# Kernel optimization log

Hardware: AMD Instinct MI355X
Metric: run time of the kernel (lower is better)

Reference implementation:

```python
import jax, jax.numpy as jnp
import numpy as np

N_TH = 32
HIDDEN = 128
BETA = 0.9
THRESH = 0.5
SCALE = 25.0
LN_EPS = 1e-5


def _spike(x):
    # forward of FastSigmoid surrogate: Heaviside
    return (x > 0).astype(x.dtype)


def _layernorm(h, g, b):
    mu = jnp.mean(h, axis=-1, keepdims=True)
    var = jnp.var(h, axis=-1, keepdims=True)
    return (h - mu) * jax.lax.rsqrt(var + LN_EPS) * g + b


def setup_inputs() -> dict:
    key = jax.random.key(0)
    ks = jax.random.split(key, 6)
    B, T = 2048, 512
    in_dim = 4 * N_TH  # 128
    x = jax.random.normal(ks[0], (B, T, 4), dtype=jnp.float32)
    W_in = jax.random.normal(ks[1], (HIDDEN, in_dim), dtype=jnp.float32) / np.sqrt(in_dim)
    b_in = jnp.zeros((HIDDEN,), dtype=jnp.float32)
    ln_g = jnp.ones((HIDDEN,), dtype=jnp.float32)
    ln_b = jnp.zeros((HIDDEN,), dtype=jnp.float32)
    W_out = jax.random.normal(ks[2], (2, HIDDEN), dtype=jnp.float32) / np.sqrt(HIDDEN)
    b_out = jnp.zeros((2,), dtype=jnp.float32)
    return {"x": x, "W_in": W_in, "b_in": b_in, "ln_g": ln_g,
            "ln_b": ln_b, "W_out": W_out, "b_out": b_out}


def reference(x, W_in, b_in, ln_g, ln_b, W_out, b_out):
    B, T, _ = x.shape
    thresholds = jnp.linspace(-3.0, 3.0, N_TH, dtype=x.dtype)  # [N_TH]
    sigma = 5.0 / N_TH
    # Gaussian threshold encoding for all 4 channels at once: [B,T,4,N_TH]
    enc = jnp.exp(-0.5 * (x[..., None] - thresholds) ** 2 / sigma ** 2)
    spikes_in = enc.reshape(B, T, 4 * N_TH)  # concat order matches channel-major
    spikes_tbd = jnp.transpose(spikes_in, (1, 0, 2))  # [T,B,128]

    mem0 = jnp.zeros((B, HIDDEN), dtype=x.dtype)
    ro0 = jnp.zeros((B, 2), dtype=x.dtype)

    def step(carry, s_t):
        mem, ro = carry
        curr = _layernorm(s_t @ W_in.T + b_in, ln_g, ln_b)
        # dropout is identity in eval mode
        mem = mem * BETA + curr * (1.0 - BETA)
        spk = _spike(mem - THRESH)
        mem = mem - spk * THRESH
        ro = ro + spk @ W_out.T + b_out
        return (mem, ro), None

    (_, readout), _ = jax.lax.scan(step, (mem0, ro0), spikes_tbd)
    return readout  # [B,2]
```

## Files before the change

### kernel.cpp

```cpp
#include <hip/hip_runtime.h>
#include <math.h>

#define HID 128
#define TT 32

typedef __attribute__((ext_vector_type(8))) short short8v;
typedef __attribute__((ext_vector_type(16))) float f32x16;

template<int CTRL, int RMASK>
__device__ __forceinline__ float dpp_add_stage(float v) {
  int s = __builtin_amdgcn_update_dpp(0, __float_as_int(v), CTRL, RMASK, 0xf, true);
  return v + __int_as_float(s);
}
__device__ __forceinline__ float wave_red_sum(float v) {
  v = dpp_add_stage<0x111, 0xf>(v);
  v = dpp_add_stage<0x112, 0xf>(v);
  v = dpp_add_stage<0x114, 0xf>(v);
  v = dpp_add_stage<0x118, 0xf>(v);
  v = dpp_add_stage<0x142, 0xa>(v);
  v = dpp_add_stage<0x143, 0xc>(v);
  return __int_as_float(__builtin_amdgcn_readlane(__float_as_int(v), 63));
}

#define REP8(F) F(0) F(1) F(2) F(3) F(4) F(5) F(6) F(7)

__device__ __forceinline__ void encode_tile(
    int tid2, int tile, unsigned int* Eh, unsigned int* El,
    const float* __restrict__ xb) {
  const int t5 = tid2 >> 2;
  const int ch = tid2 & 3;
  const float coef = (float)(-0.5 * 1024.0 / 25.0);
  float xc = xb[(tile * TT + t5) * 4 + ch];
#pragma unroll
  for (int c2 = 0; c2 < 4; ++c2) {
    unsigned int hi4[4], lo4[4];
#pragma unroll
    for (int p = 0; p < 4; ++p) {
      int j0 = c2 * 8 + p * 2;
      float th0 = fmaf((float)j0, 6.0f / 31.0f, -3.0f);
      float th1 = fmaf((float)(j0 + 1), 6.0f / 31.0f, -3.0f);
      float d0 = xc - th0, d1 = xc - th1;
      float e0 = __expf(coef * d0 * d0);
      float e1 = __expf(coef * d1 * d1);
      unsigned u0 = __float_as_uint(e0) + 0x8000u;
      unsigned u1 = __float_as_uint(e1) + 0x8000u;
      hi4[p] = __builtin_amdgcn_perm(u1, u0, 0x07060302u);
      float l0 = e0 - __uint_as_float(u0 & 0xffff0000u);
      float l1 = e1 - __uint_as_float(u1 & 0xffff0000u);
      unsigned v0 = __float_as_uint(l0) + 0x8000u;
      unsigned v1 = __float_as_uint(l1) + 0x8000u;
      lo4[p] = __builtin_amdgcn_perm(v1, v0, 0x07060302u);
    }
    int chunk = ch * 4 + c2;
    int idx = t5 * 64 + (((chunk ^ t5) & 15) << 2);
    *(uint4*)&Eh[idx] = make_uint4(hi4[0], hi4[1], hi4[2], hi4[3]);
    *(uint4*)&El[idx] = make_uint4(lo4[0], lo4[1], lo4[2], lo4[3]);
  }
}

__global__ __launch_bounds__(256) __attribute__((amdgpu_waves_per_eu(3, 3)))
void snn_mfma_kernel(
    const float* __restrict__ x, const float* __restrict__ Win,
    const float* __restrict__ b_in, const float* __restrict__ ln_g,
    const float* __restrict__ ln_b, const float* __restrict__ Wout,
    const float* __restrict__ b_out, float* __restrict__ out, int T) {
  __shared__ unsigned int Ebuf[2][TT * 64];
  __shared__ float Hn[TT * HID];
  __shared__ float red[256];
  __shared__ float bias_lds[HID];

  const int tid = threadIdx.x;
  const int w   = tid >> 6;
  const int l   = tid & 63;
  const int hh  = l >> 5;
  const int l31 = l & 31;
  const int b   = blockIdx.x;
  const int ntiles = T / TT;
  const float* xb = x + (size_t)b * (size_t)T * 4;

  const float* wrow = Win + (size_t)(32 * w + l31) * HID + hh * 8;
#define LDW(kt) short8v wh##kt, wl##kt; { \
    float tmp[8]; \
    *(float4*)&tmp[0] = *(const float4*)(wrow + (kt) * 16); \
    *(float4*)&tmp[4] = *(const float4*)(wrow + (kt) * 16 + 4); \
    _Pragma("unroll") \
    for (int e = 0; e < 8; ++e) { \
      unsigned u = __float_as_uint(tmp[e]) + 0x8000u; \
      wh##kt[e] = (short)(u >> 16); \
      float lof = tmp[e] - __uint_as_float(u & 0xffff0000u); \
      wl##kt[e] = (short)((__float_as_uint(lof) + 0x8000u) >> 16); \
    } }
  REP8(LDW)
#undef LDW

  const int srow = tid & 127;
  const float gr10 = 0.1f * ln_g[srow];
  const float br10 = 0.1f * ln_b[srow];
  const float wo0x2 = 2.0f * Wout[srow];
  const float wo1x2 = 2.0f * Wout[HID + srow];
  float mem = 0.f, cnt = 0.f;

  if (tid < 128) bias_lds[tid] = b_in[tid];
  else           encode_tile(tid - 128, 0, &Ebuf[0][0], &Ebuf[1][0], xb);
  __syncthreads();

  const unsigned int* Eh = &Ebuf[0][0];
  const unsigned int* El = &Ebuf[1][0];
  const int t5 = l31;

  for (int tau = 0; tau < ntiles; ++tau) {
#define RDB(kt) \
    short8v bh##kt = *(const short8v*)&Eh[t5 * 64 + ((((2 * (kt) + hh) ^ t5) & 15) << 2)]; \
    short8v bl##kt = *(const short8v*)&El[t5 * 64 + ((((2 * (kt) + hh) ^ t5) & 15) << 2)];

    f32x16 accA = {}, accB = {};
#define MM(kt) { RDB(kt) \
    accA = __builtin_amdgcn_mfma_f32_32x32x16_bf16(wh##kt, bh##kt, accA, 0, 0, 0); \
    accB = __builtin_amdgcn_mfma_f32_32x32x16_bf16(wh##kt, bl##kt, accB, 0, 0, 0); \
    accB = __builtin_amdgcn_mfma_f32_32x32x16_bf16(wl##kt, bh##kt, accB, 0, 0, 0); }
    REP8(MM)
#undef MM
#undef RDB

    float bb[16];
    {
      const int rb = 32 * w + 4 * hh;
      *(float4*)&bb[0]  = *(const float4*)&bias_lds[rb];
      *(float4*)&bb[4]  = *(const float4*)&bias_lds[rb + 8];
      *(float4*)&bb[8]  = *(const float4*)&bias_lds[rb + 16];
      *(float4*)&bb[12] = *(const float4*)&bias_lds[rb + 24];
    }
    float s1 = 0.f, s2 = 0.f;
#pragma unroll
    for (int r = 0; r < 16; ++r) {
      float hrv = (accA[r] + accB[r]) + bb[r];
      accA[r] = hrv;
      s1 += hrv;
      s2 = fmaf(hrv, hrv, s2);
    }
    s1 += __shfl_xor(s1, 32);
    s2 += __shfl_xor(s2, 32);
    if (l < 32) *(float2*)&red[w * 64 + 2 * l31] = make_float2(s1, s2);
    __syncthreads();

    float2 q0 = *(const float2*)&red[0 + 2 * l31];
    float2 q1 = *(const float2*)&red[64 + 2 * l31];
    float2 q2 = *(const float2*)&red[128 + 2 * l31];
    float2 q3 = *(const float2*)&red[192 + 2 * l31];
    float S1 = (q0.x + q1.x) + (q2.x + q3.x);
    float S2 = (q0.y + q1.y) + (q2.y + q3.y);
    float mu = S1 * (1.0f / 128.0f);
    float var = S2 * (1.0f / 128.0f) - mu * mu;
    float rstd = 1.0f / sqrtf(var + 1e-5f);
    float sh = -mu * rstd;

#pragma unroll
    for (int r = 0; r < 16; ++r) {
      int row = 32 * w + 4 * hh + (r & 3) + 8 * (r >> 2);
      Hn[t5 * 128 + (row ^ t5)] = fmaf(accA[r], rstd, sh);
    }
    __syncthreads();

    if (tid < 128) {
#pragma unroll 8
      for (int tt = 0; tt < TT; ++tt) {
        float hn = Hn[tt * 128 + (tid ^ tt)];
        float cc = fmaf(hn, gr10, br10);
        mem = fmaf(mem, 0.9f, cc);
        float d = (mem > 0.5f) ? 0.5f : 0.0f;
        mem -= d;
        cnt += d;
      }
    } else if (tau + 1 < ntiles) {
      encode_tile(tid - 128, tau + 1, &Ebuf[0][0], &Ebuf[1][0], xb);
    }
    __syncthreads();
  }

  float r0 = wave_red_sum(cnt * wo0x2);
  float r1 = wave_red_sum(cnt * wo1x2);
  if ((tid & 63) == 0) { red[w * 64] = r0; red[w * 64 + 1] = r1; }
  __syncthreads();
  if (tid == 0) {
    float R0 = (red[0] + red[64]) + (red[128] + red[192]);
    float R1 = (red[1] + red[65]) + (red[129] + red[193]);
    out[2 * b]     = R0 + (float)T * b_out[0];
    out[2 * b + 1] = R1 + (float)T * b_out[1];
  }
}

extern "C" void kernel_launch(void* const* d_in, const int* in_sizes, int n_in,
                              void* d_out, int out_size, void* d_ws, size_t ws_size,
                              hipStream_t stream) {
  const float* x    = (const float*)d_in[0];
  const float* Win  = (const float*)d_in[1];
  const float* bin  = (const float*)d_in[2];
  const float* lng  = (const float*)d_in[3];
  const float* lnb  = (const float*)d_in[4];
  const float* Wout = (const float*)d_in[5];
  const float* bout = (const float*)d_in[6];
  float* out = (float*)d_out;

  int B = out_size / 2;
  int T = in_sizes[0] / (B * 4);

  snn_mfma_kernel<<<dim3(B), dim3(256), 0, stream>>>(
      x, Win, bin, lng, lnb, Wout, bout, out, T);
}
```

Before: 144.3 us.

## Double-buffer encoding and overlap LIF scan with next tile's MFMA

Double-buffers the encoded spike tiles and moves the per-tile LIF scan to the start of the next iteration, so scan and encode run before the MFMA phase and one barrier per tile is removed. The Hn buffer becomes float2-paired so the scan reads two timesteps per LDS load. The Gaussian encoding switches to exp2f with a folded log2e constant and drops the round-to-nearest on the bf16 hi part (truncation instead). The MFMA hi/lo correction terms also go into a third accumulator to break the dependency chain. Costs more LDS, and changes rounding slightly.

Result: slower. 172.8 us (+19.7%).

```diff
diff --git a/kernel.cpp b/kernel.cpp
--- a/kernel.cpp
+++ b/kernel.cpp
@@ -29,7 +29,7 @@
     const float* __restrict__ xb) {
   const int t5 = tid2 >> 2;
   const int ch = tid2 & 3;
-  const float coef = (float)(-0.5 * 1024.0 / 25.0);
+  const float coef2 = (float)(-0.5 * 1024.0 / 25.0 * 1.4426950408889634);
   float xc = xb[(tile * TT + t5) * 4 + ch];
 #pragma unroll
   for (int c2 = 0; c2 < 4; ++c2) {
@@ -40,10 +40,10 @@
       float th0 = fmaf((float)j0, 6.0f / 31.0f, -3.0f);
       float th1 = fmaf((float)(j0 + 1), 6.0f / 31.0f, -3.0f);
       float d0 = xc - th0, d1 = xc - th1;
-      float e0 = __expf(coef * d0 * d0);
-      float e1 = __expf(coef * d1 * d1);
-      unsigned u0 = __float_as_uint(e0) + 0x8000u;
-      unsigned u1 = __float_as_uint(e1) + 0x8000u;
+      float e0 = exp2f(coef2 * d0 * d0);
+      float e1 = exp2f(coef2 * d1 * d1);
+      unsigned u0 = __float_as_uint(e0);
+      unsigned u1 = __float_as_uint(e1);
       hi4[p] = __builtin_amdgcn_perm(u1, u0, 0x07060302u);
       float l0 = e0 - __uint_as_float(u0 & 0xffff0000u);
       float l1 = e1 - __uint_as_float(u1 & 0xffff0000u);
@@ -64,8 +64,8 @@
     const float* __restrict__ b_in, const float* __restrict__ ln_g,
     const float* __restrict__ ln_b, const float* __restrict__ Wout,
     const float* __restrict__ b_out, float* __restrict__ out, int T) {
-  __shared__ unsigned int Ebuf[2][TT * 64];
-  __shared__ float Hn[TT * HID];
+  __shared__ unsigned int Ebuf[2][2][TT * 64];
+  __shared__ float2 Hn2[TT / 2][HID];
   __shared__ float red[256];
   __shared__ float bias_lds[HID];
 
@@ -100,40 +100,59 @@
   const float wo1x2 = 2.0f * Wout[HID + srow];
   float mem = 0.f, cnt = 0.f;
 
+  auto do_scan = [&]() {
+#pragma unroll
+    for (int tt2 = 0; tt2 < TT / 2; ++tt2) {
+      float2 hn2 = Hn2[tt2][srow ^ tt2];
+      float cc0 = fmaf(hn2.x, gr10, br10);
+      mem = fmaf(mem, 0.9f, cc0);
+      float d0 = (mem > 0.5f) ? 0.5f : 0.0f;
+      mem -= d0; cnt += d0;
+      float cc1 = fmaf(hn2.y, gr10, br10);
+      mem = fmaf(mem, 0.9f, cc1);
+      float d1 = (mem > 0.5f) ? 0.5f : 0.0f;
+      mem -= d1; cnt += d1;
+    }
+  };
+
   if (tid < 128) bias_lds[tid] = b_in[tid];
-  else           encode_tile(tid - 128, 0, &Ebuf[0][0], &Ebuf[1][0], xb);
+  else           encode_tile(tid - 128, 0, &Ebuf[0][0][0], &Ebuf[0][1][0], xb);
   __syncthreads();
 
-  const unsigned int* Eh = &Ebuf[0][0];
-  const unsigned int* El = &Ebuf[1][0];
   const int t5 = l31;
+  const int tp = t5 >> 1, par = t5 & 1;
 
   for (int tau = 0; tau < ntiles; ++tau) {
-#define RDB(kt) \
-    short8v bh##kt = *(const short8v*)&Eh[t5 * 64 + ((((2 * (kt) + hh) ^ t5) & 15) << 2)]; \
-    short8v bl##kt = *(const short8v*)&El[t5 * 64 + ((((2 * (kt) + hh) ^ t5) & 15) << 2)];
-
-    f32x16 accA = {}, accB = {};
-#define MM(kt) { RDB(kt) \
-    accA = __builtin_amdgcn_mfma_f32_32x32x16_bf16(wh##kt, bh##kt, accA, 0, 0, 0); \
-    accB = __builtin_amdgcn_mfma_f32_32x32x16_bf16(wh##kt, bl##kt, accB, 0, 0, 0); \
-    accB = __builtin_amdgcn_mfma_f32_32x32x16_bf16(wl##kt, bh##kt, accB, 0, 0, 0); }
+    const int p = tau & 1;
+    const unsigned int* Eh = &Ebuf[p][0][0];
+    const unsigned int* El = &Ebuf[p][1][0];
+
+    if (tid < 128) {
+      if (tau > 0) do_scan();
+    } else if (tau + 1 < ntiles) {
+      encode_tile(tid - 128, tau + 1, &Ebuf[p ^ 1][0][0], &Ebuf[p ^ 1][1][0], xb);
+    }
+
+    f32x16 accA = {}, accB = {}, accC = {};
+#define MM(kt) { \
+    short8v bh = *(const short8v*)&Eh[t5 * 64 + ((((2 * (kt) + hh) ^ t5) & 15) << 2)]; \
+    short8v bl = *(const short8v*)&El[t5 * 64 + ((((2 * (kt) + hh) ^ t5) & 15) << 2)]; \
+    accA = __builtin_amdgcn_mfma_f32_32x32x16_bf16(wh##kt, bh, accA, 0, 0, 0); \
+    accB = __builtin_amdgcn_mfma_f32_32x32x16_bf16(wh##kt, bl, accB, 0, 0, 0); \
+    accC = __builtin_amdgcn_mfma_f32_32x32x16_bf16(wl##kt, bh, accC, 0, 0, 0); }
     REP8(MM)
 #undef MM
-#undef RDB
 
     float bb[16];
-    {
-      const int rb = 32 * w + 4 * hh;
-      *(float4*)&bb[0]  = *(const float4*)&bias_lds[rb];
-      *(float4*)&bb[4]  = *(const float4*)&bias_lds[rb + 8];
-      *(float4*)&bb[8]  = *(const float4*)&bias_lds[rb + 16];
-      *(float4*)&bb[12] = *(const float4*)&bias_lds[rb + 24];
-    }
+    const int rb = 32 * w + 4 * hh;
+    *(float4*)&bb[0]  = *(const float4*)&bias_lds[rb];
+    *(float4*)&bb[4]  = *(const float4*)&bias_lds[rb + 8];
+    *(float4*)&bb[8]  = *(const float4*)&bias_lds[rb + 16];
+    *(float4*)&bb[12] = *(const float4*)&bias_lds[rb + 24];
     float s1 = 0.f, s2 = 0.f;
 #pragma unroll
     for (int r = 0; r < 16; ++r) {
-      float hrv = (accA[r] + accB[r]) + bb[r];
+      float hrv = (accA[r] + (accB[r] + accC[r])) + bb[r];
       accA[r] = hrv;
       s1 += hrv;
       s2 = fmaf(hrv, hrv, s2);
@@ -156,27 +175,13 @@
 
 #pragma unroll
     for (int r = 0; r < 16; ++r) {
-      int row = 32 * w + 4 * hh + (r & 3) + 8 * (r >> 2);
-      Hn[t5 * 128 + (row ^ t5)] = fmaf(accA[r], rstd, sh);
-    }
-    __syncthreads();
-
-    if (tid < 128) {
-#pragma unroll 8
-      for (int tt = 0; tt < TT; ++tt) {
-        float hn = Hn[tt * 128 + (tid ^ tt)];
-        float cc = fmaf(hn, gr10, br10);
-        mem = fmaf(mem, 0.9f, cc);
-        float d = (mem > 0.5f) ? 0.5f : 0.0f;
-        mem -= d;
-        cnt += d;
-      }
-    } else if (tau + 1 < ntiles) {
-      encode_tile(tid - 128, tau + 1, &Ebuf[0][0], &Ebuf[1][0], xb);
+      int row = rb + (r & 3) + 8 * (r >> 2);
+      ((float*)&Hn2[tp][row ^ tp])[par] = fmaf(accA[r], rstd, sh);
     }
     __syncthreads();
   }
 
+  if (tid < 128) do_scan();
   float r0 = wave_red_sum(cnt * wo0x2);
   float r1 = wave_red_sum(cnt * wo1x2);
   if ((tid & 63) == 0) { red[w * 64] = r0; red[w * 64 + 1] = r1; }
```
